# Performance work log

Hardware: AMD Instinct MI355X
Metric: run time of the kernel (lower is better)

The kernel has to match this reference:

```python
import jax, jax.numpy as jnp
import numpy as np

HIDDEN = 512
HEADS = 8
HEAD_DIM = HIDDEN // HEADS
INNER = int(HIDDEN * 4.0)
MAX_DIST = 512
LN_EPS = 1e-5


def _layernorm(x, g, b):
    mu = jnp.mean(x, axis=-1, keepdims=True)
    var = jnp.var(x, axis=-1, keepdims=True)
    return (x - mu) * jax.lax.rsqrt(var + LN_EPS) * g + b


def setup_inputs() -> dict:
    key = jax.random.key(0)
    ks = jax.random.split(key, 12)
    B, T = 4, 2048
    s = 0.02
    return {
        "x": jax.random.normal(ks[0], (B, T, HIDDEN), dtype=jnp.float32),
        "w_qkv": jax.random.normal(ks[1], (HIDDEN, 3 * HIDDEN), dtype=jnp.float32) * s,
        "b_qkv": jnp.zeros((3 * HIDDEN,), dtype=jnp.float32),
        "w_out": jax.random.normal(ks[2], (HIDDEN, HIDDEN), dtype=jnp.float32) * s,
        "b_out": jnp.zeros((HIDDEN,), dtype=jnp.float32),
        "ln1_g": jnp.ones((HIDDEN,), dtype=jnp.float32),
        "ln1_b": jnp.zeros((HIDDEN,), dtype=jnp.float32),
        "ln2_g": jnp.ones((HIDDEN,), dtype=jnp.float32),
        "ln2_b": jnp.zeros((HIDDEN,), dtype=jnp.float32),
        "w_mlp1": jax.random.normal(ks[3], (HIDDEN, INNER), dtype=jnp.float32) * s,
        "b_mlp1": jnp.zeros((INNER,), dtype=jnp.float32),
        "w_mlp2": jax.random.normal(ks[4], (INNER, HIDDEN), dtype=jnp.float32) * s,
        "b_mlp2": jnp.zeros((HIDDEN,), dtype=jnp.float32),
        "rel_table": jax.random.normal(ks[5], (2 * MAX_DIST + 1, HEADS), dtype=jnp.float32) * s,
    }


def reference(x, w_qkv, b_qkv, w_out, b_out, ln1_g, ln1_b, ln2_g, ln2_b,
              w_mlp1, b_mlp1, w_mlp2, b_mlp2, rel_table):
    B, T, C = x.shape
    scale = HEAD_DIM ** -0.5
    qkv = x @ w_qkv + b_qkv  # [B,T,3C]
    qkv = qkv.reshape(B, T, 3, HEADS, HEAD_DIM)
    q = qkv[:, :, 0].transpose(0, 2, 1, 3)  # [B,H,T,D]
    k = qkv[:, :, 1].transpose(0, 2, 1, 3)
    v = qkv[:, :, 2].transpose(0, 2, 1, 3)
    logits = jnp.einsum('bhqd,bhkd->bhqk', q, k) * scale
    # relative position bias: clamp(q_pos - k_pos) lookup -> [H,T,T]
    rel = jnp.clip(jnp.arange(T)[:, None] - jnp.arange(T)[None, :], -MAX_DIST, MAX_DIST) + MAX_DIST
    bias = rel_table[rel].transpose(2, 0, 1)  # [H,T,T]
    logits = logits + bias[None]
    attn = jax.nn.softmax(logits, axis=-1)
    out = jnp.einsum('bhqk,bhkd->bhqd', attn, v)
    out = out.transpose(0, 2, 1, 3).reshape(B, T, C)
    out = out @ w_out + b_out
    x = _layernorm(x + out, ln1_g, ln1_b)
    h = jax.nn.gelu(x @ w_mlp1 + b_mlp1, approximate=False)
    mlp_out = h @ w_mlp2 + b_mlp2
    return _layernorm(x + mlp_out, ln2_g, ln2_b)
```

## Files before the change

### kernel.cpp

```cpp
#include <hip/hip_runtime.h>
#include <hip/hip_bf16.h>

using bf16 = __hip_bfloat16;
typedef __attribute__((ext_vector_type(8))) short bf16x8;
typedef __attribute__((ext_vector_type(4))) short bf16x4;
typedef __attribute__((ext_vector_type(4))) float f32x4;

#define HIDDEN 512
#define HEADS 8
#define HDIM 64
#define INNER 2048
#define MAXD 512
#define BB 4
#define TT 2048
#define MM (BB*TT)
#define LOG2E 1.44269504088896340736f

typedef const __attribute__((address_space(1))) unsigned int* gas_u32p;
typedef __attribute__((address_space(3))) unsigned int* las_u32p;

__device__ __forceinline__ void gload_lds16(const void* g, void* l) {
    __builtin_amdgcn_global_load_lds((gas_u32p)g, (las_u32p)l, 16, 0, 0);
}
__device__ __forceinline__ short bfr(float x) {
    return (short)__bfloat16_as_ushort(__float2bfloat16(x));
}
__device__ __forceinline__ float bf2f(short u) {
    return __uint_as_float(((unsigned)(unsigned short)u) << 16);
}

__global__ __launch_bounds__(256) void prep_kernel(
    const float* __restrict__ x, const float* __restrict__ w_qkv,
    const float* __restrict__ w_out, const float* __restrict__ w1,
    const float* __restrict__ w2,
    bf16* __restrict__ xb, bf16* __restrict__ wqkv_t, bf16* __restrict__ wout_t,
    bf16* __restrict__ w1_t, bf16* __restrict__ w2_t)
{
    __shared__ float tile[32][33];
    int bid = blockIdx.x;
    if (bid < 4096) {
        int i = (bid * 256 + threadIdx.x) * 4;
        float4 v = *(const float4*)&x[i];
        bf16 o[4] = {__float2bfloat16(v.x), __float2bfloat16(v.y),
                     __float2bfloat16(v.z), __float2bfloat16(v.w)};
        *(bf16x4*)&xb[i] = *(bf16x4*)o;
        return;
    }
    bid -= 4096;
    const float* in; bf16* out; int K, N, bx, by;
    if (bid < 768)       { in = w_qkv; out = wqkv_t; K = 512;  N = 1536; bx = bid % 48; by = bid / 48; }
    else if (bid < 1024) { bid -= 768;  in = w_out; out = wout_t; K = 512;  N = 512;  bx = bid % 16; by = bid / 16; }
    else if (bid < 2048) { bid -= 1024; in = w1;   out = w1_t;   K = 512;  N = 2048; bx = bid % 64; by = bid / 64; }
    else                 { bid -= 2048; in = w2;   out = w2_t;   K = 2048; N = 512;  bx = bid % 16; by = bid / 16; }
    int lx = threadIdx.x & 31, ly = threadIdx.x >> 5;
    #pragma unroll
    for (int i = 0; i < 4; ++i)
        tile[ly + 8*i][lx] = in[(size_t)(by*32 + ly + 8*i) * N + bx*32 + lx];
    __syncthreads();
    #pragma unroll
    for (int i = 0; i < 4; ++i)
        out[(size_t)(bx*32 + ly + 8*i) * K + by*32 + lx] =
            __float2bfloat16(tile[lx][ly + 8*i]);
}

template<int EPI, int BN, int VT, int RESID>
__global__ __launch_bounds__(256) void gemm_kernel(
    const bf16* __restrict__ A, const bf16* __restrict__ BT,
    const float* __restrict__ bias, const void* __restrict__ resid,
    bf16* __restrict__ C, bf16* __restrict__ vt_out,
    int M, int N, int K)
{
    constexpr int NBF = BN / 32;
    constexpr int BBYTES = BN * 64;
    __shared__ __align__(16) bf16 As[2][128*32];
    __shared__ __align__(16) bf16 Bs[2][BN*32];
    const int tid = threadIdx.x;
    const int wid = tid >> 6;
    const int lane = tid & 63;
    const int lhi = lane >> 4, llo = lane & 15;
    const int m0 = blockIdx.x * 128, n0 = blockIdx.y * BN;
    const int wr = wid >> 1, wc = wid & 1;

    const int srow = tid >> 2;
    const int scol = ((tid & 3) ^ ((srow >> 1) & 3)) * 8;
    const bf16* Ap = A + (size_t)(m0 + srow) * K + scol;
    const bf16* Bp = BT + (size_t)(n0 + srow) * K + scol;
    const size_t step64 = (size_t)64 * K;
    const int rsw = (llo >> 1) & 3;

    f32x4 acc[4][NBF] = {};

    gload_lds16(Ap,          (char*)As + tid*16);
    gload_lds16(Ap + step64, (char*)As + 4096 + tid*16);
    gload_lds16(Bp,          (char*)Bs + tid*16);
    if (BN == 128) gload_lds16(Bp + step64, (char*)Bs + 4096 + tid*16);

    const int NK = K >> 5;
    for (int it = 0; it < NK; ++it) {
        const int p = it & 1;
        __syncthreads();
        if (it + 1 < NK) {
            const int k1 = (it + 1) << 5;
            gload_lds16(Ap + k1,          (char*)As + (p^1)*8192 + tid*16);
            gload_lds16(Ap + k1 + step64, (char*)As + (p^1)*8192 + 4096 + tid*16);
            gload_lds16(Bp + k1,          (char*)Bs + (p^1)*BBYTES + tid*16);
            if (BN == 128) gload_lds16(Bp + k1 + step64, (char*)Bs + (p^1)*BBYTES + 4096 + tid*16);
        }
        bf16x8 af[4], bfrg[NBF];
        #pragma unroll
        for (int ar = 0; ar < 4; ++ar)
            af[ar] = *(const bf16x8*)((const char*)As + p*8192 +
                       (64*wr + 16*ar + llo)*64 + ((lhi ^ rsw) << 4));
        #pragma unroll
        for (int bc = 0; bc < NBF; ++bc)
            bfrg[bc] = *(const bf16x8*)((const char*)Bs + p*BBYTES +
                       ((BN/2)*wc + 16*bc + llo)*64 + ((lhi ^ rsw) << 4));
        #pragma unroll
        for (int ar = 0; ar < 4; ++ar)
            #pragma unroll
            for (int bc = 0; bc < NBF; ++bc)
                acc[ar][bc] = __builtin_amdgcn_mfma_f32_16x16x32_bf16(
                    af[ar], bfrg[bc], acc[ar][bc], 0, 0, 0);
    }

    if (VT && n0 >= 1024) {
        #pragma unroll
        for (int ar = 0; ar < 4; ++ar) {
            const int row = m0 + 64*wr + 16*ar + 4*lhi;
            const int bq = row >> 11, t0 = row & 2047;
            #pragma unroll
            for (int bc = 0; bc < NBF; ++bc) {
                const int cv = n0 - 1024 + (BN/2)*wc + 16*bc + llo;
                const int h = cv >> 6, d = cv & 63;
                float bv = bias[n0 + (BN/2)*wc + 16*bc + llo];
                bf16x4 pk = {bfr(acc[ar][bc][0] + bv), bfr(acc[ar][bc][1] + bv),
                             bfr(acc[ar][bc][2] + bv), bfr(acc[ar][bc][3] + bv)};
                *(bf16x4*)&vt_out[(((size_t)(bq*8 + h) * 64 + d) << 11) + t0] = pk;
            }
        }
        return;
    }

    #pragma unroll
    for (int ar = 0; ar < 4; ++ar) {
        #pragma unroll
        for (int j = 0; j < 4; ++j) {
            int row = m0 + 64*wr + 16*ar + 4*lhi + j;
            #pragma unroll
            for (int bc = 0; bc < NBF; ++bc) {
                int col = n0 + (BN/2)*wc + 16*bc + llo;
                float v = acc[ar][bc][j] + bias[col];
                if (RESID == 1)
                    v += ((const float*)resid)[(size_t)row * N + col];
                if (RESID == 2)
                    v += __bfloat162float(((const bf16*)resid)[(size_t)row * N + col]);
                if (EPI == 2) {
                    float u = 0.7978845608028654f * (v + 0.044715f * v * v * v);
                    float e = __builtin_amdgcn_exp2f(u * (2.0f * LOG2E));
                    v = v * (1.0f - 1.0f / (1.0f + e));
                }
                C[(size_t)row * N + col] = __float2bfloat16(v);
            }
        }
    }
}

#define PTN (TT + 128)
__global__ __launch_bounds__(512) void attn_kernel(
    const bf16* __restrict__ qkv,
    const bf16* __restrict__ v_t,
    const float* __restrict__ rel_table,
    bf16* __restrict__ attn_out)
{
    __shared__ __align__(16) char smem[49152 + PTN*4];
    char* KsB = smem;
    char* VsB = smem + 16384;
    char* PsB = smem + 32768;
    float* PT = (float*)(smem + 49152);

    const int qt = blockIdx.x, bh = blockIdx.y;
    const int b = bh >> 3, h = bh & 7;
    const int tid = threadIdx.x, wid = tid >> 6, lane = tid & 63;
    const int lhi = lane >> 4, llo = lane & 15;
    const int gw = wid >> 2;
    const int wq = wid & 3;

    const int lo = qt*128 - (TT - 1);
    for (int i = tid; i < PTN; i += 512) {
        int idx = min(max(i + lo, -MAXD), MAXD) + MAXD;
        PT[i] = rel_table[(size_t)idx * HEADS + h] * LOG2E;
    }

    const int qb = qt * 128;
    const int q0w = qb + wq * 32;
    bf16x8 bq[2][2];
    #pragma unroll
    for (int qh = 0; qh < 2; ++qh)
        #pragma unroll
        for (int kc = 0; kc < 2; ++kc)
            bq[qh][kc] = *(const bf16x8*)&qkv[(size_t)(b*TT + q0w + qh*16 + llo) * 1536
                                              + h*64 + kc*32 + lhi*8];

    const int so = tid * 16;
    const int kg = so >> 12;
    const int kr = (so >> 7) & 31;
    const int kc0 = (((so & 127) ^ ((kr & 7) << 4)) >> 1);
    const int vd = (so >> 7) & 63;
    const int vbs = (so & 127) ^ ((vd & 7) << 4);
    const int vg = vbs >> 6;
    const int vke = (vbs & 63) >> 1;

    const bf16* kbase = qkv + (size_t)(b*TT) * 1536 + 512 + h*64;
    const bf16* vbase = v_t + (size_t)bh * 64 * TT;

    float accL[2] = {};
    f32x4 accO[2][4] = {};

    gload_lds16(kbase + (size_t)(kg*32 + kr) * 1536 + kc0, KsB + so);
    gload_lds16(vbase + (size_t)vd * TT + vg*32 + vke,     VsB + so);
    __syncthreads();

    const float cFut  = PT[min(max(-512 - lo, 0), PTN - 1)];
    const float cPast = PT[min(max( 512 - lo, 0), PTN - 1)];
    const float sc = 0.125f * LOG2E;
    const int ibq = wq*32 + llo + (TT - 1) - 4*lhi;

    for (int it = 0; it < 32; ++it) {
        const int p = it & 1;
        const int kv0 = it*64 + gw*32;
        if (it) __syncthreads();
        if (it + 1 < 32) {
            const int kn = (it + 1) * 64;
            gload_lds16(kbase + (size_t)(kn + kg*32 + kr) * 1536 + kc0, KsB + (p^1)*8192 + so);
            gload_lds16(vbase + (size_t)vd * TT + kn + vg*32 + vke,     VsB + (p^1)*8192 + so);
        }
        const char* Kb = KsB + p*8192 + gw*4096;
        const char* Vb = VsB + p*8192;

        f32x4 s[2][2] = {};
        __builtin_amdgcn_s_setprio(1);
        #pragma unroll
        for (int f = 0; f < 2; ++f) {
            const int rr = 16*f + llo;
            #pragma unroll
            for (int kc = 0; kc < 2; ++kc) {
                bf16x8 ak = *(const bf16x8*)(Kb + rr*128 + (((4*kc + lhi) ^ (rr & 7)) << 4));
                #pragma unroll
                for (int qh = 0; qh < 2; ++qh)
                    s[qh][f] = __builtin_amdgcn_mfma_f32_16x16x32_bf16(
                        ak, bq[qh][kc], s[qh][f], 0, 0, 0);
            }
        }
        __builtin_amdgcn_s_setprio(0);

        if (kv0 >= qb + 639) {
            #pragma unroll
            for (int qh = 0; qh < 2; ++qh)
                #pragma unroll
                for (int f = 0; f < 2; ++f)
                    #pragma unroll
                    for (int j = 0; j < 4; ++j)
                        s[qh][f][j] = fmaf(s[qh][f][j], sc, cFut);
        } else if (kv0 <= qb - 543) {
            #pragma unroll
            for (int qh = 0; qh < 2; ++qh)
                #pragma unroll
                for (int f = 0; f < 2; ++f)
                    #pragma unroll
                    for (int j = 0; j < 4; ++j)
                        s[qh][f][j] = fmaf(s[qh][f][j], sc, cPast);
        } else {
            const int ib = ibq - kv0;
            #pragma unroll
            for (int qh = 0; qh < 2; ++qh)
                #pragma unroll
                for (int f = 0; f < 2; ++f)
                    #pragma unroll
                    for (int j = 0; j < 4; ++j)
                        s[qh][f][j] = fmaf(s[qh][f][j], sc, PT[ib + qh*16 - 16*f - j]);
        }

        #pragma unroll
        for (int qh = 0; qh < 2; ++qh) {
            float tf = 0.f;
            #pragma unroll
            for (int f = 0; f < 2; ++f) {
                float p0 = __builtin_amdgcn_exp2f(s[qh][f][0]);
                float p1 = __builtin_amdgcn_exp2f(s[qh][f][1]);
                float p2 = __builtin_amdgcn_exp2f(s[qh][f][2]);
                float p3 = __builtin_amdgcn_exp2f(s[qh][f][3]);
                tf += (p0 + p1) + (p2 + p3);
                bf16x4 pk = {bfr(p0), bfr(p1), bfr(p2), bfr(p3)};
                *(bf16x4*)(PsB + wid*2048 + llo*128 +
                           ((qh*64 + f*32 + lhi*8) ^ ((llo & 7) << 4))) = pk;
            }
            accL[qh] += tf;
        }

        bf16x8 pf[2];
        #pragma unroll
        for (int qh = 0; qh < 2; ++qh)
            pf[qh] = *(const bf16x8*)(PsB + wid*2048 + llo*128 +
                                      ((qh*64 + lhi*16) ^ ((llo & 7) << 4)));
        __builtin_amdgcn_s_setprio(1);
        #pragma unroll
        for (int fd = 0; fd < 4; ++fd) {
            const int rv = 16*fd + llo;
            bf16x8 av = *(const bf16x8*)(Vb + rv*128 +
                         ((gw*64 + lhi*16) ^ ((rv & 7) << 4)));
            #pragma unroll
            for (int qh = 0; qh < 2; ++qh)
                accO[qh][fd] = __builtin_amdgcn_mfma_f32_16x16x32_bf16(
                    av, pf[qh], accO[qh][fd], 0, 0, 0);
        }
        __builtin_amdgcn_s_setprio(0);
    }

    #pragma unroll
    for (int qh = 0; qh < 2; ++qh) {
        accL[qh] += __shfl_xor(accL[qh], 16, 64);
        accL[qh] += __shfl_xor(accL[qh], 32, 64);
    }

    __syncthreads();
    float* xbuf = (float*)smem;
    if (gw == 1) {
        float* dst = xbuf + (size_t)(wq*64 + lane) * 34;
        #pragma unroll
        for (int qh = 0; qh < 2; ++qh)
            #pragma unroll
            for (int fd = 0; fd < 4; ++fd)
                #pragma unroll
                for (int j = 0; j < 4; ++j)
                    dst[qh*16 + fd*4 + j] = accO[qh][fd][j];
        dst[32] = accL[0]; dst[33] = accL[1];
    }
    __syncthreads();
    if (gw == 0) {
        const float* src = xbuf + (size_t)(wq*64 + lane) * 34;
        #pragma unroll
        for (int qh = 0; qh < 2; ++qh) {
            const float rl = 1.0f / (accL[qh] + src[32 + qh]);
            const int row = b*TT + q0w + qh*16 + llo;
            #pragma unroll
            for (int fd = 0; fd < 4; ++fd) {
                bf16x4 ov = {bfr((accO[qh][fd][0] + src[qh*16 + fd*4 + 0]) * rl),
                             bfr((accO[qh][fd][1] + src[qh*16 + fd*4 + 1]) * rl),
                             bfr((accO[qh][fd][2] + src[qh*16 + fd*4 + 2]) * rl),
                             bfr((accO[qh][fd][3] + src[qh*16 + fd*4 + 3]) * rl)};
                *(bf16x4*)&attn_out[(size_t)row * HIDDEN + h*64 + 16*fd + 4*lhi] = ov;
            }
        }
    }
}

template<int WB>
__global__ __launch_bounds__(256) void ln_kernel(
    const bf16* __restrict__ in,
    const float* __restrict__ g, const float* __restrict__ bb,
    float* __restrict__ of, bf16* __restrict__ ob)
{
    int row = blockIdx.x * 4 + (threadIdx.x >> 6);
    int lane = threadIdx.x & 63;
    const bf16* pa = in + (size_t)row * HIDDEN + lane * 8;
    bf16x8 v8 = *(const bf16x8*)pa;
    float v[8];
    float s = 0.f, sq = 0.f;
    #pragma unroll
    for (int j = 0; j < 8; ++j) {
        v[j] = bf2f(v8[j]);
        s += v[j]; sq += v[j] * v[j];
    }
    #pragma unroll
    for (int d = 1; d < 64; d <<= 1) {
        s  += __shfl_xor(s,  d, 64);
        sq += __shfl_xor(sq, d, 64);
    }
    float mean = s * (1.f / HIDDEN);
    float var  = sq * (1.f / HIDDEN) - mean * mean;
    float rstd = rsqrtf(var + 1e-5f);
    float o[8];
    #pragma unroll
    for (int j = 0; j < 8; ++j) {
        int col = lane * 8 + j;
        o[j] = (v[j] - mean) * rstd * g[col] + bb[col];
    }
    if (WB) {
        bf16x8 ov;
        #pragma unroll
        for (int j = 0; j < 8; ++j) ov[j] = bfr(o[j]);
        *(bf16x8*)&ob[(size_t)row * HIDDEN + lane * 8] = ov;
    } else {
        float4 o0 = {o[0], o[1], o[2], o[3]};
        float4 o1 = {o[4], o[5], o[6], o[7]};
        *(float4*)&of[(size_t)row * HIDDEN + lane * 8]     = o0;
        *(float4*)&of[(size_t)row * HIDDEN + lane * 8 + 4] = o1;
    }
}

extern "C" void kernel_launch(void* const* d_in, const int* in_sizes, int n_in,
                              void* d_out, int out_size, void* d_ws, size_t ws_size,
                              hipStream_t stream) {
    const float* x     = (const float*)d_in[0];
    const float* w_qkv = (const float*)d_in[1];
    const float* b_qkv = (const float*)d_in[2];
    const float* w_out = (const float*)d_in[3];
    const float* b_out = (const float*)d_in[4];
    const float* ln1_g = (const float*)d_in[5];
    const float* ln1_b = (const float*)d_in[6];
    const float* ln2_g = (const float*)d_in[7];
    const float* ln2_b = (const float*)d_in[8];
    const float* w1    = (const float*)d_in[9];
    const float* b1    = (const float*)d_in[10];
    const float* w2    = (const float*)d_in[11];
    const float* b2    = (const float*)d_in[12];
    const float* rel   = (const float*)d_in[13];
    float* out = (float*)d_out;

    char* ws = (char*)d_ws;
    bf16*  xb     = (bf16*)(ws + 0);
    bf16*  wqkv_t = (bf16*)(ws + 8388608);
    bf16*  wout_t = (bf16*)(ws + 9961472);
    bf16*  w1_t   = (bf16*)(ws + 10485760);
    bf16*  w2_t   = (bf16*)(ws + 12582912);
    bf16*  qkv    = (bf16*)(ws + 14680064);
    bf16*  v_t    = (bf16*)(ws + 39845888);
    bf16*  attn_o = (bf16*)(ws + 48234496);
    bf16*  proj   = (bf16*)(ws + 56623104);
    bf16*  h      = (bf16*)(ws + 14680064);
    bf16*  x1b    = (bf16*)(ws + 90177536);

    prep_kernel<<<7168, 256, 0, stream>>>(x, w_qkv, w_out, w1, w2,
                                          xb, wqkv_t, wout_t, w1_t, w2_t);
    gemm_kernel<0,128,1,0><<<dim3(MM/128, 1536/128), 256, 0, stream>>>(
        xb, wqkv_t, b_qkv, nullptr, qkv, v_t, MM, 1536, 512);
    attn_kernel<<<dim3(TT/128, BB*HEADS), 512, 0, stream>>>(qkv, v_t, rel, attn_o);
    gemm_kernel<0,64,0,1><<<dim3(MM/128, 512/64), 256, 0, stream>>>(
        attn_o, wout_t, b_out, x, proj, nullptr, MM, 512, 512);
    ln_kernel<1><<<MM/4, 256, 0, stream>>>(proj, ln1_g, ln1_b, nullptr, x1b);
    gemm_kernel<2,128,0,0><<<dim3(MM/128, 2048/128), 256, 0, stream>>>(
        x1b, w1_t, b1, nullptr, h, nullptr, MM, 2048, 512);
    gemm_kernel<0,64,0,2><<<dim3(MM/128, 512/64), 256, 0, stream>>>(
        h, w2_t, b2, x1b, proj, nullptr, MM, 512, 2048);
    ln_kernel<0><<<MM/4, 256, 0, stream>>>(proj, ln2_g, ln2_b, out, nullptr);
}
```

Measured before the change: 177.8 us.

## Compute softmax row sums via MFMA and widen MLP1 GEMM tile to 256

In the attention kernel, the per-row softmax denominator is now accumulated by an extra MFMA of a ones vector against the probability fragments. This replaces the scalar adds and the cross-lane shuffle reduction. The GEMM staging is generalized through a lambda so BN=256 works, and the MLP1 GEMM is launched with 128x256 tiles to raise data reuse per block. The trade-off is extra MFMA work per iteration, plus higher register and LDS use for the wider tile, which may cut occupancy. Row sums are now taken from the bf16-rounded probabilities rather than the fp32 values.

```diff
diff --git a/kernel.cpp b/kernel.cpp
--- a/kernel.cpp
+++ b/kernel.cpp
@@ -71,6 +71,7 @@
     int M, int N, int K)
 {
     constexpr int NBF = BN / 32;
+    constexpr int NBS = BN / 64;
     constexpr int BBYTES = BN * 64;
     __shared__ __align__(16) bf16 As[2][128*32];
     __shared__ __align__(16) bf16 Bs[2][BN*32];
@@ -90,22 +91,22 @@
 
     f32x4 acc[4][NBF] = {};
 
-    gload_lds16(Ap,          (char*)As + tid*16);
-    gload_lds16(Ap + step64, (char*)As + 4096 + tid*16);
-    gload_lds16(Bp,          (char*)Bs + tid*16);
-    if (BN == 128) gload_lds16(Bp + step64, (char*)Bs + 4096 + tid*16);
+    auto STAGE = [&](int k1, int bi) {
+        #pragma unroll
+        for (int rr = 0; rr < 2; ++rr)
+            gload_lds16(Ap + k1 + rr*step64, (char*)As + bi*8192 + rr*4096 + tid*16);
+        #pragma unroll
+        for (int rr = 0; rr < NBS; ++rr)
+            gload_lds16(Bp + k1 + rr*step64, (char*)Bs + bi*BBYTES + rr*4096 + tid*16);
+    };
+
+    STAGE(0, 0);
 
     const int NK = K >> 5;
     for (int it = 0; it < NK; ++it) {
         const int p = it & 1;
         __syncthreads();
-        if (it + 1 < NK) {
-            const int k1 = (it + 1) << 5;
-            gload_lds16(Ap + k1,          (char*)As + (p^1)*8192 + tid*16);
-            gload_lds16(Ap + k1 + step64, (char*)As + (p^1)*8192 + 4096 + tid*16);
-            gload_lds16(Bp + k1,          (char*)Bs + (p^1)*BBYTES + tid*16);
-            if (BN == 128) gload_lds16(Bp + k1 + step64, (char*)Bs + (p^1)*BBYTES + 4096 + tid*16);
-        }
+        if (it + 1 < NK) STAGE((it + 1) << 5, p^1);
         bf16x8 af[4], bfrg[NBF];
         #pragma unroll
         for (int ar = 0; ar < 4; ++ar)
@@ -201,6 +202,10 @@
             bq[qh][kc] = *(const bf16x8*)&qkv[(size_t)(b*TT + q0w + qh*16 + llo) * 1536
                                               + h*64 + kc*32 + lhi*8];
 
+    bf16x8 aones;
+    #pragma unroll
+    for (int i = 0; i < 8; ++i) aones[i] = (short)0x3F80;
+
     const int so = tid * 16;
     const int kg = so >> 12;
     const int kr = (so >> 7) & 31;
@@ -213,7 +218,7 @@
     const bf16* kbase = qkv + (size_t)(b*TT) * 1536 + 512 + h*64;
     const bf16* vbase = v_t + (size_t)bh * 64 * TT;
 
-    float accL[2] = {};
+    f32x4 accLf[2] = {};
     f32x4 accO[2][4] = {};
 
     gload_lds16(kbase + (size_t)(kg*32 + kr) * 1536 + kc0, KsB + so);
@@ -282,19 +287,16 @@
 
         #pragma unroll
         for (int qh = 0; qh < 2; ++qh) {
-            float tf = 0.f;
             #pragma unroll
             for (int f = 0; f < 2; ++f) {
                 float p0 = __builtin_amdgcn_exp2f(s[qh][f][0]);
                 float p1 = __builtin_amdgcn_exp2f(s[qh][f][1]);
                 float p2 = __builtin_amdgcn_exp2f(s[qh][f][2]);
                 float p3 = __builtin_amdgcn_exp2f(s[qh][f][3]);
-                tf += (p0 + p1) + (p2 + p3);
                 bf16x4 pk = {bfr(p0), bfr(p1), bfr(p2), bfr(p3)};
                 *(bf16x4*)(PsB + wid*2048 + llo*128 +
                            ((qh*64 + f*32 + lhi*8) ^ ((llo & 7) << 4))) = pk;
             }
-            accL[qh] += tf;
         }
 
         bf16x8 pf[2];
@@ -313,13 +315,11 @@
                 accO[qh][fd] = __builtin_amdgcn_mfma_f32_16x16x32_bf16(
                     av, pf[qh], accO[qh][fd], 0, 0, 0);
         }
+        #pragma unroll
+        for (int qh = 0; qh < 2; ++qh)
+            accLf[qh] = __builtin_amdgcn_mfma_f32_16x16x32_bf16(
+                aones, pf[qh], accLf[qh], 0, 0, 0);
         __builtin_amdgcn_s_setprio(0);
-    }
-
-    #pragma unroll
-    for (int qh = 0; qh < 2; ++qh) {
-        accL[qh] += __shfl_xor(accL[qh], 16, 64);
-        accL[qh] += __shfl_xor(accL[qh], 32, 64);
     }
 
     __syncthreads();
@@ -333,14 +333,14 @@
                 #pragma unroll
                 for (int j = 0; j < 4; ++j)
                     dst[qh*16 + fd*4 + j] = accO[qh][fd][j];
-        dst[32] = accL[0]; dst[33] = accL[1];
+        dst[32] = accLf[0][0]; dst[33] = accLf[1][0];
     }
     __syncthreads();
     if (gw == 0) {
         const float* src = xbuf + (size_t)(wq*64 + lane) * 34;
         #pragma unroll
         for (int qh = 0; qh < 2; ++qh) {
-            const float rl = 1.0f / (accL[qh] + src[32 + qh]);
+            const float rl = 1.0f / (accLf[qh][0] + src[32 + qh]);
             const int row = b*TT + q0w + qh*16 + llo;
             #pragma unroll
             for (int fd = 0; fd < 4; ++fd) {
@@ -438,7 +438,7 @@
     gemm_kernel<0,64,0,1><<<dim3(MM/128, 512/64), 256, 0, stream>>>(
         attn_o, wout_t, b_out, x, proj, nullptr, MM, 512, 512);
     ln_kernel<1><<<MM/4, 256, 0, stream>>>(proj, ln1_g, ln1_b, nullptr, x1b);
-    gemm_kernel<2,128,0,0><<<dim3(MM/128, 2048/128), 256, 0, stream>>>(
+    gemm_kernel<2,256,0,0><<<dim3(MM/128, 2048/256), 256, 0, stream>>>(
         x1b, w1_t, b1, nullptr, h, nullptr, MM, 2048, 512);
     gemm_kernel<0,64,0,2><<<dim3(MM/128, 512/64), 256, 0, stream>>>(
         h, w2_t, b2, x1b, proj, nullptr, MM, 512, 2048);
```

Measured after the change: 189.2 us. 1.06x slower.
